# Optimization experiments

Hardware: AMD Instinct MI355X
Metric: run time of the kernel (lower is better)

Reference implementation:

```python
import jax, jax.numpy as jnp
import numpy as np

D, E, N, DD, K = 1024, 2048, 16, 64, 4  # d_model, d_inner, d_state, dt_rank, d_conv
B, L = 2, 1024
EPS = 1e-5


def setup_inputs() -> dict:
    key = jax.random.key(0)
    ks = jax.random.split(key, 12)
    f = lambda k, s, scale=0.02: (jax.random.normal(k, s, jnp.float32) * scale)
    return dict(
        resid=jax.random.normal(ks[0], (B, L, D), jnp.float32),
        workplace_h=jnp.zeros((B, E, N), jnp.float32),
        norm_w=jnp.ones((D,), jnp.float32),
        skip_w=f(ks[1], (E, D)),
        in_w=f(ks[2], (E, D)),
        conv_w=f(ks[3], (E, 1, K), 0.2),
        conv_b=jnp.zeros((E,), jnp.float32),
        wd1=f(ks[4], (DD, E)),
        wd2_w=f(ks[5], (E, DD)),
        wd2_b=jnp.zeros((E,), jnp.float32),
        wb=f(ks[6], (N, E)),
        wc=f(ks[7], (N, E)),
        A_log=f(ks[8], (E, N), 1.0),
        W_D=jnp.ones((E,), jnp.float32),
        out_w=f(ks[9], (D, E)),
    )


def reference(resid, workplace_h, norm_w, skip_w, in_w, conv_w, conv_b,
              wd1, wd2_w, wd2_b, wb, wc, A_log, W_D, out_w):
    # RMSNorm
    x = resid * jax.lax.rsqrt(jnp.mean(resid ** 2, -1, keepdims=True) + EPS) * norm_w
    skip = x @ skip_w.T                      # [B,L,E]
    xi = x @ in_w.T                          # [B,L,E]
    # depthwise causal conv1d (torch pads both sides then slices to L; equivalent to left-pad K-1)
    xc = jnp.swapaxes(xi, 1, 2)              # [B,E,L]
    xc = jax.lax.conv_general_dilated(
        xc, conv_w, window_strides=(1,), padding=[(K - 1, 0)],
        feature_group_count=E, dimension_numbers=('NCH', 'OIH', 'NCH'))
    xc = xc + conv_b[None, :, None]
    x2 = jax.nn.silu(jnp.swapaxes(xc, 1, 2))  # [B,L,E]

    A = -jnp.exp(A_log)                       # [E,N]
    delta = jax.nn.softplus((x2 @ wd1.T) @ wd2_w.T + wd2_b)   # [B,L,E]
    A_bar = jnp.exp(delta[..., None] * A)                      # [B,L,E,N]
    Bm = x2 @ wb.T                                             # [B,L,N]
    B_bar = delta[..., None] * Bm[:, :, None, :]               # [B,L,E,N]
    Cm = x2 @ wc.T                                             # [B,L,N]

    def step(h, inp):
        a, b_, xl, cl = inp                   # [B,E,N],[B,E,N],[B,E],[B,N]
        h = a * h + b_ * xl[..., None]
        y = jnp.einsum('ben,bn->be', h, cl)
        return h, y

    h0 = jnp.zeros_like(workplace_h)          # workplace_h is zeroed (h[:] = 0)
    xs = (jnp.swapaxes(A_bar, 0, 1), jnp.swapaxes(B_bar, 0, 1),
          jnp.swapaxes(x2, 0, 1), jnp.swapaxes(Cm, 0, 1))
    _, ys = jax.lax.scan(step, h0, xs)        # ys: [L,B,E]
    y = jnp.swapaxes(ys, 0, 1)                # [B,L,E]

    y = (y + x2 * W_D) * jax.nn.silu(skip)
    return resid + y @ out_w.T
```

## Files before the change

kernel.cpp:

```cpp
#include <hip/hip_runtime.h>
#include <math.h>

#define Dm 1024
#define Em 2048
#define Nm 16
#define DDm 64
#define Bb 2
#define Lm 1024
#define Mrows (Bb*Lm)
#define NCH 32
#define CLEN 32
#define KS 16

typedef __attribute__((ext_vector_type(8))) short bf16x8;
typedef __attribute__((ext_vector_type(4))) float f32x4;
typedef unsigned int u32;
typedef unsigned short u16;

__device__ __forceinline__ u16 f2bf(float f) {
    union { float f; u32 u; } v; v.f = f;
    u32 r = v.u + 0x7fffu + ((v.u >> 16) & 1u);
    return (u16)(r >> 16);
}

__device__ __forceinline__ void async_copy16(const void* g, void* l) {
    __builtin_amdgcn_global_load_lds(
        (const __attribute__((address_space(1))) u32*)g,
        (__attribute__((address_space(3))) u32*)l,
        16, 0, 0);
}

__global__ __launch_bounds__(256) void rmsnorm_kernel(const float* __restrict__ resid,
                                                      const float* __restrict__ w,
                                                      u16* __restrict__ x) {
    int row = blockIdx.x;
    const float* r = resid + (size_t)row * Dm;
    float s = 0.f;
    for (int i = threadIdx.x; i < Dm; i += 256) { float v = r[i]; s += v * v; }
    __shared__ float red[4];
    for (int off = 32; off; off >>= 1) s += __shfl_down(s, off, 64);
    if ((threadIdx.x & 63) == 0) red[threadIdx.x >> 6] = s;
    __syncthreads();
    if (threadIdx.x == 0) {
        float t = red[0] + red[1] + red[2] + red[3];
        red[0] = rsqrtf(t / (float)Dm + 1e-5f);
    }
    __syncthreads();
    float sc = red[0];
    u16* xo = x + (size_t)row * Dm;
    for (int i = threadIdx.x; i < Dm; i += 256) xo[i] = f2bf(r[i] * sc * w[i]);
}

__global__ __launch_bounds__(256) void prep_all_kernel(const float* __restrict__ skip_w,
                                                       const float* __restrict__ in_w,
                                                       const float* __restrict__ out_w,
                                                       const float* __restrict__ wd2_w,
                                                       const float* __restrict__ wb,
                                                       const float* __restrict__ wc,
                                                       const float* __restrict__ wd1,
                                                       u16* __restrict__ skip_w_bf,
                                                       u16* __restrict__ in_w_bf,
                                                       u16* __restrict__ out_w_bf,
                                                       u16* __restrict__ wd2_bf,
                                                       u16* __restrict__ wtb) {
    const int R0 = 2097152, R1 = 4194304, R2 = 6291456, R3 = 6422528, R4 = 6684672;
    int i = blockIdx.x * 256 + threadIdx.x;
    if (i < R0) skip_w_bf[i] = f2bf(skip_w[i]);
    else if (i < R1) in_w_bf[i - R0] = f2bf(in_w[i - R0]);
    else if (i < R2) out_w_bf[i - R1] = f2bf(out_w[i - R1]);
    else if (i < R3) wd2_bf[i - R2] = f2bf(wd2_w[i - R2]);
    else if (i < R4) {
        int j = i - R3;
        int c = j >> 11, k = j & 2047;
        float v = 0.f;
        if (c < 16) v = wb[(size_t)c * Em + k];
        else if (c < 32) v = wc[(size_t)(c - 16) * Em + k];
        else if (c < 96) v = wd1[(size_t)(c - 32) * Em + k];
        wtb[j] = f2bf(v);
    }
}

__global__ __launch_bounds__(256) void gemm_bf16(const u16* __restrict__ A,
                                                 const u16* __restrict__ W,
                                                 const float* __restrict__ bias,
                                                 const float* __restrict__ addend,
                                                 float* __restrict__ C,
                                                 float* __restrict__ C2, int split,
                                                 int M, int N, int K, int act) {
    __shared__ __align__(16) u16 As[128 * 32];
    __shared__ __align__(16) u16 Ws[128 * 32];
    int tid = threadIdx.x;
    int lane = tid & 63, wave = tid >> 6;
    int bm = blockIdx.y * 128, bn = blockIdx.x * 128;
    int lm = lane & 15, lq = lane >> 4;
    int wm = (wave & 1) * 64, wn = (wave >> 1) * 64;

    f32x4 acc[4][4] = {};
    int ldrow = (lane >> 2);
    int ldchunk = (lane & 3) * 8;

    for (int k0 = 0; k0 < K; k0 += 32) {
        #pragma unroll
        for (int i = 0; i < 2; ++i) {
            int rbase = i * 64 + wave * 16;
            async_copy16(A + (size_t)(bm + rbase + ldrow) * K + k0 + ldchunk, &As[rbase * 32]);
            async_copy16(W + (size_t)(bn + rbase + ldrow) * K + k0 + ldchunk, &Ws[rbase * 32]);
        }
        __syncthreads();
        bf16x8 a[4], b[4];
        #pragma unroll
        for (int mi = 0; mi < 4; ++mi)
            a[mi] = *(const bf16x8*)&As[(wm + mi * 16 + lm) * 32 + lq * 8];
        #pragma unroll
        for (int nj = 0; nj < 4; ++nj)
            b[nj] = *(const bf16x8*)&Ws[(wn + nj * 16 + lm) * 32 + lq * 8];
        #pragma unroll
        for (int mi = 0; mi < 4; ++mi)
            #pragma unroll
            for (int nj = 0; nj < 4; ++nj)
                acc[mi][nj] = __builtin_amdgcn_mfma_f32_16x16x32_bf16(a[mi], b[nj], acc[mi][nj], 0, 0, 0);
        __syncthreads();
    }

    #pragma unroll
    for (int nj = 0; nj < 4; ++nj) {
        int col = bn + wn + nj * 16 + lm;
        float bv = bias ? bias[col] : 0.f;
        float* Cp = C; int colw = col; int ldc = N;
        if (C2) { ldc = split; if (col >= split) { Cp = C2; colw = col - split; } }
        #pragma unroll
        for (int mi = 0; mi < 4; ++mi) {
            #pragma unroll
            for (int r = 0; r < 4; ++r) {
                int row = bm + wm + mi * 16 + lq * 4 + r;
                float v = acc[mi][nj][r] + bv;
                if (act == 1) v = (v > 20.f) ? v : log1pf(expf(v));
                size_t off = (size_t)row * ldc + colw;
                if (addend) v += addend[off];
                Cp[off] = v;
            }
        }
    }
}

__global__ __launch_bounds__(256) void small_gemm_mfma(const u16* __restrict__ A,
                                                       const u16* __restrict__ W,
                                                       float* __restrict__ Cp) {
    __shared__ __align__(16) u16 As[128 * 32];
    __shared__ __align__(16) u16 Ws[128 * 32];
    int tid = threadIdx.x;
    int lane = tid & 63, wave = tid >> 6;
    int bm = blockIdx.x * 128;
    int k0base = blockIdx.y * (Em / KS);
    int lm = lane & 15, lq = lane >> 4;
    int wm = (wave & 1) * 64, wn = (wave >> 1) * 64;

    f32x4 acc[4][4] = {};
    int ldrow = (lane >> 2);
    int ldchunk = (lane & 3) * 8;

    #pragma unroll
    for (int kk = 0; kk < (Em / KS) / 32; ++kk) {
        int k0 = k0base + kk * 32;
        #pragma unroll
        for (int i = 0; i < 2; ++i) {
            int rbase = i * 64 + wave * 16;
            async_copy16(A + (size_t)(bm + rbase + ldrow) * Em + k0 + ldchunk, &As[rbase * 32]);
            async_copy16(W + (size_t)(rbase + ldrow) * Em + k0 + ldchunk, &Ws[rbase * 32]);
        }
        __syncthreads();
        bf16x8 a[4], b[4];
        #pragma unroll
        for (int mi = 0; mi < 4; ++mi)
            a[mi] = *(const bf16x8*)&As[(wm + mi * 16 + lm) * 32 + lq * 8];
        #pragma unroll
        for (int nj = 0; nj < 4; ++nj)
            b[nj] = *(const bf16x8*)&Ws[(wn + nj * 16 + lm) * 32 + lq * 8];
        #pragma unroll
        for (int mi = 0; mi < 4; ++mi)
            #pragma unroll
            for (int nj = 0; nj < 4; ++nj)
                acc[mi][nj] = __builtin_amdgcn_mfma_f32_16x16x32_bf16(a[mi], b[nj], acc[mi][nj], 0, 0, 0);
        __syncthreads();
    }

    float* Co = Cp + (size_t)blockIdx.y * (Mrows * 128);
    #pragma unroll
    for (int nj = 0; nj < 4; ++nj) {
        int col = wn + nj * 16 + lm;
        #pragma unroll
        for (int mi = 0; mi < 4; ++mi) {
            #pragma unroll
            for (int r = 0; r < 4; ++r) {
                int row = bm + wm + mi * 16 + lq * 4 + r;
                Co[(size_t)row * 128 + col] = acc[mi][nj][r];
            }
        }
    }
}

__global__ __launch_bounds__(256) void small_reduce_kernel(const float* __restrict__ Cp,
                                                           float* __restrict__ Bm,
                                                           float* __restrict__ Cm,
                                                           u16* __restrict__ d1) {
    int idx = blockIdx.x * 256 + threadIdx.x;
    int row = idx >> 7, col = idx & 127;
    float s = 0.f;
    #pragma unroll
    for (int ks = 0; ks < KS; ++ks) s += Cp[(size_t)ks * (Mrows * 128) + idx];
    if (col < 16) Bm[(size_t)row * 16 + col] = s;
    else if (col < 32) Cm[(size_t)row * 16 + (col - 16)] = s;
    else if (col < 96) d1[(size_t)row * 64 + (col - 32)] = f2bf(s);
}

__global__ __launch_bounds__(256) void conv_silu_kernel(const float* __restrict__ xi,
                                                        const float* __restrict__ cw,
                                                        const float* __restrict__ cb,
                                                        float* __restrict__ x2,
                                                        u16* __restrict__ x2b, int total) {
    int idx = blockIdx.x * 256 + threadIdx.x;
    if (idx >= total) return;
    int e = idx & (Em - 1);
    int l = (idx >> 11) & (Lm - 1);
    const float* base = xi + idx;
    float w0 = cw[e * 4 + 0], w1 = cw[e * 4 + 1], w2 = cw[e * 4 + 2], w3 = cw[e * 4 + 3];
    float acc = cb[e];
    if (l >= 3) acc += w0 * base[-3 * Em];
    if (l >= 2) acc += w1 * base[-2 * Em];
    if (l >= 1) acc += w2 * base[-1 * Em];
    acc += w3 * base[0];
    float v = acc / (1.f + __expf(-acc));
    x2[idx] = v;
    x2b[idx] = f2bf(v);
}

__global__ __launch_bounds__(256) void scan1_kernel(const float* __restrict__ delta,
                                                    const float* __restrict__ x2,
                                                    const float* __restrict__ Bm,
                                                    const float* __restrict__ A_log,
                                                    float* __restrict__ h_end,
                                                    float* __restrict__ P) {
    int e = (blockIdx.x & 7) * 256 + threadIdx.x;
    int bc = blockIdx.x >> 3;
    int b = bc & 1, c = bc >> 1;
    float A[16];
    {
        const float4* al = (const float4*)(A_log + e * 16);
        float4 q0 = al[0], q1 = al[1], q2 = al[2], q3 = al[3];
        A[0]=-expf(q0.x); A[1]=-expf(q0.y); A[2]=-expf(q0.z); A[3]=-expf(q0.w);
        A[4]=-expf(q1.x); A[5]=-expf(q1.y); A[6]=-expf(q1.z); A[7]=-expf(q1.w);
        A[8]=-expf(q2.x); A[9]=-expf(q2.y); A[10]=-expf(q2.z); A[11]=-expf(q2.w);
        A[12]=-expf(q3.x); A[13]=-expf(q3.y); A[14]=-expf(q3.z); A[15]=-expf(q3.w);
    }
    float h[16], Pr[16];
    #pragma unroll
    for (int k = 0; k < 16; ++k) { h[k] = 0.f; Pr[k] = 1.f; }

    int l0 = c * CLEN;
    const float* dp = delta + ((size_t)(b * Lm + l0)) * Em + e;
    const float* xp = x2    + ((size_t)(b * Lm + l0)) * Em + e;
    const float* bp = Bm    + ((size_t)(b * Lm + l0)) * Nm;

    float d_n = dp[0], x_n = xp[0];
    float4 b0n = *(const float4*)(bp + 0), b1n = *(const float4*)(bp + 4);
    float4 b2n = *(const float4*)(bp + 8), b3n = *(const float4*)(bp + 12);

    #pragma unroll 1
    for (int l = 0; l < CLEN; ++l) {
        float d = d_n, xv = x_n;
        float4 b0 = b0n, b1 = b1n, b2 = b2n, b3 = b3n;
        if (l < CLEN - 1) {
            d_n = dp[(size_t)(l + 1) * Em]; x_n = xp[(size_t)(l + 1) * Em];
            const float* nb = bp + (size_t)(l + 1) * Nm;
            b0n = *(const float4*)(nb); b1n = *(const float4*)(nb + 4);
            b2n = *(const float4*)(nb + 8); b3n = *(const float4*)(nb + 12);
        }
        float dx = d * xv;
        float bb[16] = {b0.x,b0.y,b0.z,b0.w, b1.x,b1.y,b1.z,b1.w,
                        b2.x,b2.y,b2.z,b2.w, b3.x,b3.y,b3.z,b3.w};
        #pragma unroll
        for (int k = 0; k < 16; ++k) {
            float a = __expf(d * A[k]);
            h[k] = a * h[k] + bb[k] * dx;
            Pr[k] *= a;
        }
    }
    size_t base = (((size_t)c * 2 + b) * 16) * 2048 + e;
    #pragma unroll
    for (int k = 0; k < 16; ++k) {
        h_end[base + k * 2048] = h[k];
        P[base + k * 2048] = Pr[k];
    }
}

__global__ __launch_bounds__(256) void scan2_kernel(float* __restrict__ h_end,
                                                    const float* __restrict__ P) {
    int T = blockIdx.x * 256 + threadIdx.x;
    float hi = 0.f;
    float he_n = h_end[T], p_n = P[T];
    #pragma unroll 1
    for (int c = 0; c < NCH; ++c) {
        float he = he_n, p = p_n;
        if (c < NCH - 1) {
            he_n = h_end[(size_t)(c + 1) * 65536 + T];
            p_n  = P[(size_t)(c + 1) * 65536 + T];
        }
        float hnew = fmaf(p, hi, he);
        h_end[(size_t)c * 65536 + T] = hi;
        hi = hnew;
    }
}

__global__ __launch_bounds__(256) void scan3_kernel(const float* __restrict__ delta,
                                                    const float* __restrict__ x2,
                                                    const float* __restrict__ Bm,
                                                    const float* __restrict__ Cm,
                                                    const float* __restrict__ A_log,
                                                    const float* __restrict__ h_init,
                                                    const float* __restrict__ skip,
                                                    const float* __restrict__ W_D,
                                                    u16* __restrict__ yb) {
    int e = (blockIdx.x & 7) * 256 + threadIdx.x;
    int bc = blockIdx.x >> 3;
    int b = bc & 1, c = bc >> 1;
    float A[16];
    {
        const float4* al = (const float4*)(A_log + e * 16);
        float4 q0 = al[0], q1 = al[1], q2 = al[2], q3 = al[3];
        A[0]=-expf(q0.x); A[1]=-expf(q0.y); A[2]=-expf(q0.z); A[3]=-expf(q0.w);
        A[4]=-expf(q1.x); A[5]=-expf(q1.y); A[6]=-expf(q1.z); A[7]=-expf(q1.w);
        A[8]=-expf(q2.x); A[9]=-expf(q2.y); A[10]=-expf(q2.z); A[11]=-expf(q2.w);
        A[12]=-expf(q3.x); A[13]=-expf(q3.y); A[14]=-expf(q3.z); A[15]=-expf(q3.w);
    }
    float h[16];
    {
        size_t base = (((size_t)c * 2 + b) * 16) * 2048 + e;
        #pragma unroll
        for (int k = 0; k < 16; ++k) h[k] = h_init[base + k * 2048];
    }
    float wd = W_D[e];

    int l0 = c * CLEN;
    const float* dp = delta + ((size_t)(b * Lm + l0)) * Em + e;
    const float* xp = x2    + ((size_t)(b * Lm + l0)) * Em + e;
    const float* sp = skip  + ((size_t)(b * Lm + l0)) * Em + e;
    const float* bp = Bm    + ((size_t)(b * Lm + l0)) * Nm;
    const float* cp = Cm    + ((size_t)(b * Lm + l0)) * Nm;
    u16* yp = yb + ((size_t)(b * Lm + l0)) * Em + e;

    float d_n = dp[0], x_n = xp[0], s_n = sp[0];
    float4 b0n = *(const float4*)(bp + 0), b1n = *(const float4*)(bp + 4);
    float4 b2n = *(const float4*)(bp + 8), b3n = *(const float4*)(bp + 12);
    float4 c0n = *(const float4*)(cp + 0), c1n = *(const float4*)(cp + 4);
    float4 c2n = *(const float4*)(cp + 8), c3n = *(const float4*)(cp + 12);

    #pragma unroll 1
    for (int l = 0; l < CLEN; ++l) {
        float d = d_n, xv = x_n, sv = s_n;
        float4 b0 = b0n, b1 = b1n, b2 = b2n, b3 = b3n;
        float4 c0 = c0n, c1 = c1n, c2 = c2n, c3 = c3n;
        if (l < CLEN - 1) {
            d_n = dp[(size_t)(l + 1) * Em]; x_n = xp[(size_t)(l + 1) * Em];
            s_n = sp[(size_t)(l + 1) * Em];
            const float* nb = bp + (size_t)(l + 1) * Nm;
            b0n = *(const float4*)(nb); b1n = *(const float4*)(nb + 4);
            b2n = *(const float4*)(nb + 8); b3n = *(const float4*)(nb + 12);
            const float* nc = cp + (size_t)(l + 1) * Nm;
            c0n = *(const float4*)(nc); c1n = *(const float4*)(nc + 4);
            c2n = *(const float4*)(nc + 8); c3n = *(const float4*)(nc + 12);
        }
        float dx = d * xv;
        float bb[16] = {b0.x,b0.y,b0.z,b0.w, b1.x,b1.y,b1.z,b1.w,
                        b2.x,b2.y,b2.z,b2.w, b3.x,b3.y,b3.z,b3.w};
        float cc[16] = {c0.x,c0.y,c0.z,c0.w, c1.x,c1.y,c1.z,c1.w,
                        c2.x,c2.y,c2.z,c2.w, c3.x,c3.y,c3.z,c3.w};
        float yv = 0.f;
        #pragma unroll
        for (int k = 0; k < 16; ++k) {
            float a = __expf(d * A[k]);
            h[k] = a * h[k] + bb[k] * dx;
            yv += h[k] * cc[k];
        }
        float sig = 1.f / (1.f + __expf(-sv));
        yp[(size_t)l * Em] = f2bf((yv + xv * wd) * (sv * sig));
    }
}

extern "C" void kernel_launch(void* const* d_in, const int* in_sizes, int n_in,
                              void* d_out, int out_size, void* d_ws, size_t ws_size,
                              hipStream_t stream) {
    const float* resid  = (const float*)d_in[0];
    const float* norm_w = (const float*)d_in[2];
    const float* skip_w = (const float*)d_in[3];
    const float* in_w   = (const float*)d_in[4];
    const float* conv_w = (const float*)d_in[5];
    const float* conv_b = (const float*)d_in[6];
    const float* wd1    = (const float*)d_in[7];
    const float* wd2_w  = (const float*)d_in[8];
    const float* wd2_b  = (const float*)d_in[9];
    const float* wb     = (const float*)d_in[10];
    const float* wc     = (const float*)d_in[11];
    const float* A_log  = (const float*)d_in[12];
    const float* W_D    = (const float*)d_in[13];
    const float* out_w  = (const float*)d_in[14];
    float* out = (float*)d_out;

    float* ws = (float*)d_ws;
    float* region0 = ws; ws += 3 * 1024 * 1024;
    u16* x_bf      = (u16*)region0;
    u16* skip_w_bf = (u16*)(region0 + 1024 * 1024);
    u16* in_w_bf   = (u16*)(region0 + 2 * 1024 * 1024);
    float* h_endb  = region0;
    u16* out_w_bf  = (u16*)ws; ws += 1024 * 1024;
    u16* wd2_bf    = (u16*)ws; ws += 65536;
    u16* d1_bf     = (u16*)ws; ws += 65536;
    u16* wtb       = (u16*)ws; ws += 131072;
    float* Pbuf    = ws; ws += 2 * 1024 * 1024;
    float* Cpart   = ws; ws += (size_t)KS * Mrows * 128;
    float* skip    = ws; ws += (size_t)Mrows * Em;
    float* xi      = ws; ws += (size_t)Mrows * Em;
    float* x2      = ws; ws += (size_t)Mrows * Em;
    u16* x2_bf     = (u16*)ws; ws += (size_t)Mrows * Em / 2;
    u16* yb_bf     = (u16*)ws; ws += (size_t)Mrows * Em / 2;
    float* Bmb     = ws; ws += (size_t)Mrows * Nm;
    float* Cmb     = ws; ws += (size_t)Mrows * Nm;
    float* delta   = xi;

    const int M = Mrows;

    prep_all_kernel<<<6684672 / 256, 256, 0, stream>>>(
        skip_w, in_w, out_w, wd2_w, wb, wc, wd1,
        skip_w_bf, in_w_bf, out_w_bf, wd2_bf, wtb);

    rmsnorm_kernel<<<M, 256, 0, stream>>>(resid, norm_w, x_bf);

    gemm_bf16<<<dim3(2 * Em / 128, M / 128), 256, 0, stream>>>(
        x_bf, skip_w_bf, nullptr, nullptr, skip, xi, Em, M, 2 * Em, Dm, 0);

    conv_silu_kernel<<<(M * Em) / 256, 256, 0, stream>>>(xi, conv_w, conv_b, x2, x2_bf, M * Em);

    small_gemm_mfma<<<dim3(M / 128, KS), 256, 0, stream>>>(x2_bf, wtb, Cpart);
    small_reduce_kernel<<<(M * 128) / 256, 256, 0, stream>>>(Cpart, Bmb, Cmb, d1_bf);

    gemm_bf16<<<dim3(Em / 128, M / 128), 256, 0, stream>>>(
        d1_bf, wd2_bf, wd2_b, nullptr, delta, nullptr, 0, M, Em, DDm, 1);

    scan1_kernel<<<Bb * NCH * 8, 256, 0, stream>>>(delta, x2, Bmb, A_log, h_endb, Pbuf);
    scan2_kernel<<<65536 / 256, 256, 0, stream>>>(h_endb, Pbuf);
    scan3_kernel<<<Bb * NCH * 8, 256, 0, stream>>>(delta, x2, Bmb, Cmb, A_log, h_endb,
                                                   skip, W_D, yb_bf);

    gemm_bf16<<<dim3(Dm / 128, M / 128), 256, 0, stream>>>(
        yb_bf, out_w_bf, nullptr, resid, out, nullptr, 0, M, Dm, Em, 0);
}
```

Baseline: 323.7 us.

## Shrink GEMM N-tile to 64 and split-K the output projection

Replaces the 128x128 GEMM with a 128x64-tile variant to double the block count for all three dense GEMMs. It also adds a split-K of 4 for the output projection, writing partials into the dead skip buffer and summing them with the residual in a new reduce kernel. The aim is better CU occupancy on the small-grid GEMMs, in particular the out projection, which had only 128 blocks. The cost is less reuse per tile, extra partial-sum traffic and one more kernel launch.

```diff
diff --git a/kernel.cpp b/kernel.cpp
--- a/kernel.cpp
+++ b/kernel.cpp
@@ -11,6 +11,7 @@
 #define NCH 32
 #define CLEN 32
 #define KS 16
+#define KSO 4
 
 typedef __attribute__((ext_vector_type(8))) short bf16x8;
 typedef __attribute__((ext_vector_type(4))) float f32x4;
@@ -80,54 +81,60 @@
     }
 }
 
-__global__ __launch_bounds__(256) void gemm_bf16(const u16* __restrict__ A,
-                                                 const u16* __restrict__ W,
-                                                 const float* __restrict__ bias,
-                                                 const float* __restrict__ addend,
-                                                 float* __restrict__ C,
-                                                 float* __restrict__ C2, int split,
-                                                 int M, int N, int K, int act) {
+__global__ __launch_bounds__(256) void gemm64(const u16* __restrict__ A,
+                                              const u16* __restrict__ W,
+                                              const float* __restrict__ bias,
+                                              const float* __restrict__ addend,
+                                              float* __restrict__ C,
+                                              float* __restrict__ C2, int split,
+                                              int M, int N, int lda, int klen, int act) {
     __shared__ __align__(16) u16 As[128 * 32];
-    __shared__ __align__(16) u16 Ws[128 * 32];
+    __shared__ __align__(16) u16 Ws[64 * 32];
     int tid = threadIdx.x;
     int lane = tid & 63, wave = tid >> 6;
-    int bm = blockIdx.y * 128, bn = blockIdx.x * 128;
+    int bm = blockIdx.y * 128, bn = blockIdx.x * 64;
+    int kbase = blockIdx.z * klen;
     int lm = lane & 15, lq = lane >> 4;
-    int wm = (wave & 1) * 64, wn = (wave >> 1) * 64;
-
-    f32x4 acc[4][4] = {};
+    int wm = (wave & 1) * 64, wn = (wave >> 1) * 32;
+
+    f32x4 acc[4][2] = {};
     int ldrow = (lane >> 2);
     int ldchunk = (lane & 3) * 8;
 
-    for (int k0 = 0; k0 < K; k0 += 32) {
+    for (int k0 = kbase; k0 < kbase + klen; k0 += 32) {
         #pragma unroll
         for (int i = 0; i < 2; ++i) {
             int rbase = i * 64 + wave * 16;
-            async_copy16(A + (size_t)(bm + rbase + ldrow) * K + k0 + ldchunk, &As[rbase * 32]);
-            async_copy16(W + (size_t)(bn + rbase + ldrow) * K + k0 + ldchunk, &Ws[rbase * 32]);
+            async_copy16(A + (size_t)(bm + rbase + ldrow) * lda + k0 + ldchunk, &As[rbase * 32]);
+        }
+        {
+            int rbase = wave * 16;
+            async_copy16(W + (size_t)(bn + rbase + ldrow) * lda + k0 + ldchunk, &Ws[rbase * 32]);
         }
         __syncthreads();
-        bf16x8 a[4], b[4];
+        bf16x8 a[4], b[2];
         #pragma unroll
         for (int mi = 0; mi < 4; ++mi)
             a[mi] = *(const bf16x8*)&As[(wm + mi * 16 + lm) * 32 + lq * 8];
         #pragma unroll
-        for (int nj = 0; nj < 4; ++nj)
+        for (int nj = 0; nj < 2; ++nj)
             b[nj] = *(const bf16x8*)&Ws[(wn + nj * 16 + lm) * 32 + lq * 8];
         #pragma unroll
         for (int mi = 0; mi < 4; ++mi)
             #pragma unroll
-            for (int nj = 0; nj < 4; ++nj)
+            for (int nj = 0; nj < 2; ++nj)
                 acc[mi][nj] = __builtin_amdgcn_mfma_f32_16x16x32_bf16(a[mi], b[nj], acc[mi][nj], 0, 0, 0);
         __syncthreads();
     }
 
-    #pragma unroll
-    for (int nj = 0; nj < 4; ++nj) {
+    int ldc = C2 ? split : N;
+    float* Cz = C + (size_t)blockIdx.z * M * ldc;
+    #pragma unroll
+    for (int nj = 0; nj < 2; ++nj) {
         int col = bn + wn + nj * 16 + lm;
         float bv = bias ? bias[col] : 0.f;
-        float* Cp = C; int colw = col; int ldc = N;
-        if (C2) { ldc = split; if (col >= split) { Cp = C2; colw = col - split; } }
+        float* Cp = Cz; int colw = col;
+        if (C2 && col >= split) { Cp = C2; colw = col - split; }
         #pragma unroll
         for (int mi = 0; mi < 4; ++mi) {
             #pragma unroll
@@ -141,6 +148,22 @@
             }
         }
     }
+}
+
+__global__ __launch_bounds__(256) void out_reduce_kernel(const float* __restrict__ part,
+                                                         const float* __restrict__ resid,
+                                                         float* __restrict__ out) {
+    int idx = blockIdx.x * 256 + threadIdx.x;
+    const float4* r4 = (const float4*)resid;
+    const float4* p4 = (const float4*)part;
+    float4 s = r4[idx];
+    const int plane = Mrows * Dm / 4;
+    #pragma unroll
+    for (int ks = 0; ks < KSO; ++ks) {
+        float4 p = p4[(size_t)ks * plane + idx];
+        s.x += p.x; s.y += p.y; s.z += p.z; s.w += p.w;
+    }
+    ((float4*)out)[idx] = s;
 }
 
 __global__ __launch_bounds__(256) void small_gemm_mfma(const u16* __restrict__ A,
@@ -425,6 +448,7 @@
     float* Bmb     = ws; ws += (size_t)Mrows * Nm;
     float* Cmb     = ws; ws += (size_t)Mrows * Nm;
     float* delta   = xi;
+    float* OutPart = skip;
 
     const int M = Mrows;
 
@@ -434,22 +458,23 @@
 
     rmsnorm_kernel<<<M, 256, 0, stream>>>(resid, norm_w, x_bf);
 
-    gemm_bf16<<<dim3(2 * Em / 128, M / 128), 256, 0, stream>>>(
-        x_bf, skip_w_bf, nullptr, nullptr, skip, xi, Em, M, 2 * Em, Dm, 0);
+    gemm64<<<dim3(2 * Em / 64, M / 128, 1), 256, 0, stream>>>(
+        x_bf, skip_w_bf, nullptr, nullptr, skip, xi, Em, M, 2 * Em, Dm, Dm, 0);
 
     conv_silu_kernel<<<(M * Em) / 256, 256, 0, stream>>>(xi, conv_w, conv_b, x2, x2_bf, M * Em);
 
     small_gemm_mfma<<<dim3(M / 128, KS), 256, 0, stream>>>(x2_bf, wtb, Cpart);
     small_reduce_kernel<<<(M * 128) / 256, 256, 0, stream>>>(Cpart, Bmb, Cmb, d1_bf);
 
-    gemm_bf16<<<dim3(Em / 128, M / 128), 256, 0, stream>>>(
-        d1_bf, wd2_bf, wd2_b, nullptr, delta, nullptr, 0, M, Em, DDm, 1);
+    gemm64<<<dim3(Em / 64, M / 128, 1), 256, 0, stream>>>(
+        d1_bf, wd2_bf, wd2_b, nullptr, delta, nullptr, 0, M, Em, DDm, DDm, 1);
 
     scan1_kernel<<<Bb * NCH * 8, 256, 0, stream>>>(delta, x2, Bmb, A_log, h_endb, Pbuf);
     scan2_kernel<<<65536 / 256, 256, 0, stream>>>(h_endb, Pbuf);
     scan3_kernel<<<Bb * NCH * 8, 256, 0, stream>>>(delta, x2, Bmb, Cmb, A_log, h_endb,
                                                    skip, W_D, yb_bf);
 
-    gemm_bf16<<<dim3(Dm / 128, M / 128), 256, 0, stream>>>(
-        yb_bf, out_w_bf, nullptr, resid, out, nullptr, 0, M, Dm, Em, 0);
-}
+    gemm64<<<dim3(Dm / 64, M / 128, KSO), 256, 0, stream>>>(
+        yb_bf, out_w_bf, nullptr, nullptr, OutPart, nullptr, 0, M, Dm, Em, Em / KSO, 0);
+    out_reduce_kernel<<<(M * Dm / 4) / 256, 256, 0, stream>>>(OutPart, resid, out);
+}
```

Result: faster. 280.1 us (-13.5%).
